# Kernel optimization log

Hardware: AMD Instinct MI355X
Metric: run time of the kernel (lower is better)

Reference implementation:

```python
import jax, jax.numpy as jnp
import numpy as np


def _reverse_padded(x, lengths):
    # x: [T, B, D]; reverse each sequence within its own length (packed-seq semantics)
    T = x.shape[0]
    t = jnp.arange(T)[:, None]                                   # [T, 1]
    idx = jnp.where(t < lengths[None, :], lengths[None, :] - 1 - t, t)  # [T, B]
    return jnp.take_along_axis(x, idx[:, :, None], axis=0)


def _lstm_dir(x, w_ih, w_hh, b):
    # single-direction LSTM, torch gate order (i, f, g, o). x: [T, B, Din]
    T, B, _ = x.shape
    H = w_hh.shape[1]
    xg = jnp.einsum('tbi,gi->tbg', x, w_ih) + b  # precompute input projections [T,B,4H]

    def step(carry, g_x):
        h, c = carry
        g = g_x + h @ w_hh.T
        i, f, gc, o = jnp.split(g, 4, axis=-1)
        c = jax.nn.sigmoid(f) * c + jax.nn.sigmoid(i) * jnp.tanh(gc)
        h = jax.nn.sigmoid(o) * jnp.tanh(c)
        return (h, c), h

    h0 = jnp.zeros((B, H), x.dtype)
    _, hs = jax.lax.scan(step, (h0, h0), xg)
    return hs  # [T, B, H]


def _bilstm_layer(x, lengths, wf, whf, bf, wr, whr, br):
    fwd = _lstm_dir(x, wf, whf, bf)
    rev = _reverse_padded(_lstm_dir(_reverse_padded(x, lengths), wr, whr, br), lengths)
    return jnp.concatenate([fwd, rev], axis=-1)  # [T, B, 2H]


def setup_inputs() -> dict:
    T, B, D, H = 256, 128, 300, 256
    key = jax.random.key(0)
    ks = jax.random.split(key, 24)
    stdv = 1.0 / np.sqrt(H)

    def u(k, shape):
        return jax.random.uniform(k, shape, jnp.float32, -stdv, stdv)

    inp = {
        'x': jax.random.normal(ks[0], (T, B, D), jnp.float32),
        'lengths': jax.random.randint(ks[1], (B,), 1, T + 1),
        # layer 0 forward / reverse
        'w_ih_l0': u(ks[2], (4 * H, D)), 'w_hh_l0': u(ks[3], (4 * H, H)),
        'b_ih_l0': u(ks[4], (4 * H,)), 'b_hh_l0': u(ks[5], (4 * H,)),
        'w_ih_l0r': u(ks[6], (4 * H, D)), 'w_hh_l0r': u(ks[7], (4 * H, H)),
        'b_ih_l0r': u(ks[8], (4 * H,)), 'b_hh_l0r': u(ks[9], (4 * H,)),
        # layer 1 forward / reverse (input dim 2H)
        'w_ih_l1': u(ks[10], (4 * H, 2 * H)), 'w_hh_l1': u(ks[11], (4 * H, H)),
        'b_ih_l1': u(ks[12], (4 * H,)), 'b_hh_l1': u(ks[13], (4 * H,)),
        'w_ih_l1r': u(ks[14], (4 * H, 2 * H)), 'w_hh_l1r': u(ks[15], (4 * H, H)),
        'b_ih_l1r': u(ks[16], (4 * H,)), 'b_hh_l1r': u(ks[17], (4 * H,)),
        # attention MLP + context vector
        'mlp_w': u(ks[18], (2 * H, 2 * H)),
        'mlp_b': u(ks[19], (2 * H,)),
        'ctx': jax.random.normal(ks[20], (2 * H,), jnp.float32) * 0.1,
    }
    return inp


def reference(x, lengths, w_ih_l0, w_hh_l0, b_ih_l0, b_hh_l0,
              w_ih_l0r, w_hh_l0r, b_ih_l0r, b_hh_l0r,
              w_ih_l1, w_hh_l1, b_ih_l1, b_hh_l1,
              w_ih_l1r, w_hh_l1r, b_ih_l1r, b_hh_l1r,
              mlp_w, mlp_b, ctx):
    lengths = jnp.maximum(lengths, 1)
    h1 = _bilstm_layer(x, lengths, w_ih_l0, w_hh_l0, b_ih_l0 + b_hh_l0,
                       w_ih_l0r, w_hh_l0r, b_ih_l0r + b_hh_l0r)
    h2 = _bilstm_layer(h1, lengths, w_ih_l1, w_hh_l1, b_ih_l1 + b_hh_l1,
                       w_ih_l1r, w_hh_l1r, b_ih_l1r + b_hh_l1r)
    out = h2.transpose(1, 0, 2)                                  # [B, T, 2H]
    ann = jnp.tanh(jnp.einsum('btd,ed->bte', out, mlp_w) + mlp_b)  # [B, T, 2H]
    scores = ann @ ctx                                           # [B, T]
    T = out.shape[1]
    mask = jnp.arange(T)[None, :] < lengths[:, None]             # [B, T]
    w = jax.nn.softmax(jnp.where(mask, scores, -1e9), axis=1)    # masked softmax over time
    return jnp.einsum('bt,btd->bd', w, out)                      # [B, 2H]
```

## Files before the change

### kernel.cpp

```cpp
#include <hip/hip_runtime.h>


#define T_ 256
#define B_ 128
#define D_ 300
#define H_ 256
#define G4H 1024
#define H2 512
#define TC 64
#define LDK 40
#define LDA 264

typedef __attribute__((ext_vector_type(8))) short bf16x8;
typedef __attribute__((ext_vector_type(4))) short short4v;
typedef __attribute__((ext_vector_type(4))) float f32x4;

#define MFMA16(a, b, c) __builtin_amdgcn_mfma_f32_16x16x32_bf16(a, b, c, 0, 0, 0)

__device__ __forceinline__ float sigf(float x) { return 1.f / (1.f + __expf(-x)); }
__device__ __forceinline__ float tanhfast(float x) { return 2.f / (1.f + __expf(-2.f * x)) - 1.f; }

__device__ __forceinline__ short hi_bf16(float x) {
  return (short)(__float_as_uint(x) >> 16);
}
__device__ __forceinline__ short lo_bf16(float x) {
  float lo = x - __uint_as_float(__float_as_uint(x) & 0xFFFF0000u);
  return (short)(__float_as_uint(lo) >> 16);
}

__device__ __forceinline__ void split_f4(const float4 v, short* hp, short* lp) {
  short4v h, l;
  h.x = hi_bf16(v.x); l.x = lo_bf16(v.x);
  h.y = hi_bf16(v.y); l.y = lo_bf16(v.y);
  h.z = hi_bf16(v.z); l.z = lo_bf16(v.z);
  h.w = hi_bf16(v.w); l.w = lo_bf16(v.w);
  *(short4v*)hp = h;
  *(short4v*)lp = l;
}

__device__ __forceinline__ void split8(const float4 v0, const float4 v1,
                                       bf16x8* hp, bf16x8* lp) {
  bf16x8 h, l;
  h[0] = hi_bf16(v0.x); l[0] = lo_bf16(v0.x);
  h[1] = hi_bf16(v0.y); l[1] = lo_bf16(v0.y);
  h[2] = hi_bf16(v0.z); l[2] = lo_bf16(v0.z);
  h[3] = hi_bf16(v0.w); l[3] = lo_bf16(v0.w);
  h[4] = hi_bf16(v1.x); l[4] = lo_bf16(v1.x);
  h[5] = hi_bf16(v1.y); l[5] = lo_bf16(v1.y);
  h[6] = hi_bf16(v1.z); l[6] = lo_bf16(v1.z);
  h[7] = hi_bf16(v1.w); l[7] = lo_bf16(v1.w);
  *hp = h; *lp = l;
}

__global__ __launch_bounds__(256, 2) void proj_gemm2(
    const float* __restrict__ X,
    const float* __restrict__ W0, const float* __restrict__ W1,
    const float* __restrict__ b1f, const float* __restrict__ b2f,
    const float* __restrict__ b1r, const float* __restrict__ b2r,
    float* __restrict__ C0, float* __restrict__ C1,
    int N, int K, const int* __restrict__ lengths, int t0)
{
  __shared__ short Xh[128 * LDK], Xl[128 * LDK];
  __shared__ short Wh[128 * LDK], Wl[128 * LDK];
  const int rev = blockIdx.z;
  const float* __restrict__ W = rev ? W1 : W0;
  const float* __restrict__ bias1 = rev ? b1r : b1f;
  const float* __restrict__ bias2 = rev ? b2r : b2f;
  float* __restrict__ C = rev ? C1 : C0;

  const int tid = threadIdx.x;
  const int m0 = blockIdx.y * 128, n0 = blockIdx.x * 128;
  const int s_step = t0 + blockIdx.y;

  const int sr = tid >> 3;
  const int sc = (tid & 7) * 4;
  const float* px[4];
  const float* pw[4];
#pragma unroll
  for (int p = 0; p < 4; p++) {
    const int r = sr + p * 32;
    int ss = s_step;
    if (rev) {
      int lb = lengths[r]; if (lb < 1) lb = 1;
      ss = (s_step < lb) ? (lb - 1 - s_step) : s_step;
    }
    px[p] = X + (size_t)(ss * 128 + r) * K;
    pw[p] = W + (size_t)(n0 + r) * K;
  }

  const int lane = tid & 63, w = tid >> 6;
  const int mb = (w & 1) * 64, nb = (w >> 1) * 64;
  const int r16 = lane & 15, quad = lane >> 4;

  f32x4 acc[4][4];
#pragma unroll
  for (int i = 0; i < 4; i++)
#pragma unroll
    for (int j = 0; j < 4; j++) acc[i][j] = (f32x4){0.f, 0.f, 0.f, 0.f};

  for (int k0 = 0; k0 < K; k0 += 32) {
    const int gk = k0 + sc;
    const bool kin = (gk < K);
#pragma unroll
    for (int p = 0; p < 4; p++) {
      float4 xv = {0.f, 0.f, 0.f, 0.f}, wv = {0.f, 0.f, 0.f, 0.f};
      if (kin) { xv = *(const float4*)(px[p] + gk); wv = *(const float4*)(pw[p] + gk); }
      const int ro = (sr + p * 32) * LDK + sc;
      split_f4(xv, &Xh[ro], &Xl[ro]);
      split_f4(wv, &Wh[ro], &Wl[ro]);
    }
    __syncthreads();

    bf16x8 ah[4], al[4], bh[4], bl[4];
#pragma unroll
    for (int mt = 0; mt < 4; mt++) {
      const int ro = (mb + mt * 16 + r16) * LDK + quad * 8;
      ah[mt] = *(const bf16x8*)&Xh[ro];
      al[mt] = *(const bf16x8*)&Xl[ro];
    }
#pragma unroll
    for (int nt = 0; nt < 4; nt++) {
      const int ro = (nb + nt * 16 + r16) * LDK + quad * 8;
      bh[nt] = *(const bf16x8*)&Wh[ro];
      bl[nt] = *(const bf16x8*)&Wl[ro];
    }
#pragma unroll
    for (int mt = 0; mt < 4; mt++)
#pragma unroll
      for (int nt = 0; nt < 4; nt++) {
        acc[mt][nt] = __builtin_amdgcn_mfma_f32_16x16x32_bf16(ah[mt], bh[nt], acc[mt][nt], 0, 0, 0);
        acc[mt][nt] = __builtin_amdgcn_mfma_f32_16x16x32_bf16(ah[mt], bl[nt], acc[mt][nt], 0, 0, 0);
        acc[mt][nt] = __builtin_amdgcn_mfma_f32_16x16x32_bf16(al[mt], bh[nt], acc[mt][nt], 0, 0, 0);
      }
    __syncthreads();
  }

  float bsum[4];
#pragma unroll
  for (int nt = 0; nt < 4; nt++) {
    const int col = n0 + nb + nt * 16 + r16;
    bsum[nt] = bias1[col] + bias2[col];
  }
#pragma unroll
  for (int mt = 0; mt < 4; mt++) {
    const int row = m0 + mb + mt * 16 + quad * 4;
#pragma unroll
    for (int nt = 0; nt < 4; nt++) {
      const int col = n0 + nb + nt * 16 + r16;
      float* Cp = C + (size_t)row * N + col;
#pragma unroll
      for (int reg = 0; reg < 4; reg++)
        Cp[(size_t)reg * N] = acc[mt][nt][reg] + bsum[nt];
    }
  }
}

__global__ __launch_bounds__(256, 2) void attn_gemm(
    const float* __restrict__ X, const float* __restrict__ W,
    const float* __restrict__ mlp_b, const float* __restrict__ ctx,
    float* __restrict__ scores, int M, int N, int K)
{
  __shared__ short Xh[128 * LDK], Xl[128 * LDK];
  __shared__ short Wh[128 * LDK], Wl[128 * LDK];
  const int tid = threadIdx.x;
  const int m0 = blockIdx.y * 128, n0 = blockIdx.x * 128;

  const int sr = tid >> 3;
  const int sc = (tid & 7) * 4;
  const float* px[4];
  const float* pw[4];
#pragma unroll
  for (int p = 0; p < 4; p++) {
    px[p] = X + (size_t)(m0 + sr + p * 32) * K;
    pw[p] = W + (size_t)(n0 + sr + p * 32) * K;
  }

  const int lane = tid & 63, w = tid >> 6;
  const int mb = (w & 1) * 64, nb = (w >> 1) * 64;
  const int r16 = lane & 15, quad = lane >> 4;

  f32x4 acc[4][4];
#pragma unroll
  for (int i = 0; i < 4; i++)
#pragma unroll
    for (int j = 0; j < 4; j++) acc[i][j] = (f32x4){0.f, 0.f, 0.f, 0.f};

  for (int k0 = 0; k0 < K; k0 += 32) {
    const int gk = k0 + sc;
#pragma unroll
    for (int p = 0; p < 4; p++) {
      float4 xv = *(const float4*)(px[p] + gk);
      float4 wv = *(const float4*)(pw[p] + gk);
      const int ro = (sr + p * 32) * LDK + sc;
      split_f4(xv, &Xh[ro], &Xl[ro]);
      split_f4(wv, &Wh[ro], &Wl[ro]);
    }
    __syncthreads();

    bf16x8 ah[4], al[4], bh[4], bl[4];
#pragma unroll
    for (int mt = 0; mt < 4; mt++) {
      const int ro = (mb + mt * 16 + r16) * LDK + quad * 8;
      ah[mt] = *(const bf16x8*)&Xh[ro];
      al[mt] = *(const bf16x8*)&Xl[ro];
    }
#pragma unroll
    for (int nt = 0; nt < 4; nt++) {
      const int ro = (nb + nt * 16 + r16) * LDK + quad * 8;
      bh[nt] = *(const bf16x8*)&Wh[ro];
      bl[nt] = *(const bf16x8*)&Wl[ro];
    }
#pragma unroll
    for (int mt = 0; mt < 4; mt++)
#pragma unroll
      for (int nt = 0; nt < 4; nt++) {
        acc[mt][nt] = __builtin_amdgcn_mfma_f32_16x16x32_bf16(ah[mt], bh[nt], acc[mt][nt], 0, 0, 0);
        acc[mt][nt] = __builtin_amdgcn_mfma_f32_16x16x32_bf16(ah[mt], bl[nt], acc[mt][nt], 0, 0, 0);
        acc[mt][nt] = __builtin_amdgcn_mfma_f32_16x16x32_bf16(al[mt], bh[nt], acc[mt][nt], 0, 0, 0);
      }
    __syncthreads();
  }

  float bb4[4], cc4[4];
#pragma unroll
  for (int nt = 0; nt < 4; nt++) {
    const int col = n0 + nb + nt * 16 + r16;
    bb4[nt] = mlp_b[col];
    cc4[nt] = ctx[col];
  }
#pragma unroll
  for (int mt = 0; mt < 4; mt++) {
#pragma unroll
    for (int reg = 0; reg < 4; reg++) {
      float ssum = 0.f;
#pragma unroll
      for (int nt = 0; nt < 4; nt++)
        ssum += tanhfast(acc[mt][nt][reg] + bb4[nt]) * cc4[nt];
      ssum += __shfl_xor(ssum, 1);
      ssum += __shfl_xor(ssum, 2);
      ssum += __shfl_xor(ssum, 4);
      ssum += __shfl_xor(ssum, 8);
      if (r16 == 0)
        atomicAdd(&scores[m0 + mb + mt * 16 + quad * 4 + reg], ssum);
    }
  }
}

__global__ __launch_bounds__(256, 1) void lstm_rec(
    const float* __restrict__ xgF, const float* __restrict__ xgR,
    const float* __restrict__ whF, const float* __restrict__ whR,
    const int* __restrict__ lengths, float* __restrict__ hout,
    float* __restrict__ ring, float* __restrict__ bbuf, float* __restrict__ cbuf,
    int t0)
{
  __shared__ short Ah[16 * LDA];
  __shared__ short Al[16 * LDA];
  __shared__ float gbuf[8 * 128];

  const int tid = threadIdx.x;
  const int blk = blockIdx.x;
  const int s = blk >> 5;
  const int d = (blk >> 4) & 1;
  const int g = blk & 15;
  const float* __restrict__ xg = d ? xgR : xgF;
  const float* __restrict__ wh = d ? whR : whF;

  const int lane = tid & 63;
  const int w = tid >> 6;
  const int r16 = lane & 15, quad = lane >> 4;

  const int cb = tid >> 5;
  const int hl = tid & 31;
  const int b = g * 8 + cb;
  const int hdim = s * 32 + hl;
  const int k0 = hl * 8;

  bf16x8 bh[2][8], bl[2][8];
#pragma unroll
  for (int nt = 0; nt < 2; nt++)
#pragma unroll
    for (int kt = 0; kt < 8; kt++) {
      const float* wr = wh + (size_t)(w * 256 + s * 32 + nt * 16 + r16) * 256
                           + kt * 32 + quad * 8;
      float4 v0 = *(const float4*)(wr);
      float4 v1 = *(const float4*)(wr + 4);
      split8(v0, v1, &bh[nt][kt], &bl[nt][kt]);
    }

  {
    int* za = (int*)(Ah + 8 * LDA);
    int* zb = (int*)(Al + 8 * LDA);
    for (int i = tid; i < (8 * LDA) / 2; i += 256) { za[i] = 0; zb[i] = 0; }
  }

  float c;
  if (t0 == 0) {
    int* za = (int*)Ah;
    int* zb = (int*)Al;
    for (int i = tid; i < (8 * LDA) / 2; i += 256) { za[i] = 0; zb[i] = 0; }
    c = 0.f;
  } else {
    const float* src = bbuf + ((size_t)d * 128 + g * 8 + cb) * 256 + k0;
    float4 v0 = *(const float4*)src;
    float4 v1 = *(const float4*)(src + 4);
    bf16x8 hv, lv;
    split8(v0, v1, &hv, &lv);
    *(bf16x8*)&Ah[cb * LDA + k0] = hv;
    *(bf16x8*)&Al[cb * LDA + k0] = lv;
    c = cbuf[((size_t)d * 128 + b) * 256 + hdim];
  }
  int lb = lengths[b]; if (lb < 1) lb = 1;

  const float* xr0 = xg + (size_t)b * 1024 + hdim;
  float x0 = xr0[0], x1 = xr0[256], x2 = xr0[512], x3 = xr0[768];
  __syncthreads();

  const int tend = t0 + TC;
  for (int t = t0; t < tend; t++) {
    const int slot = t - t0;
    const bool last = (t == tend - 1);

    f32x4 aH0 = {0.f,0.f,0.f,0.f}, aM0 = {0.f,0.f,0.f,0.f}, aL0 = {0.f,0.f,0.f,0.f};
    f32x4 aH1 = {0.f,0.f,0.f,0.f}, aM1 = {0.f,0.f,0.f,0.f}, aL1 = {0.f,0.f,0.f,0.f};
#pragma unroll
    for (int kt = 0; kt < 8; kt++) {
      const int ro = r16 * LDA + kt * 32 + quad * 8;
      bf16x8 ahf = *(const bf16x8*)&Ah[ro];
      bf16x8 alf = *(const bf16x8*)&Al[ro];
      aH0 = MFMA16(ahf, bh[0][kt], aH0);
      aM0 = MFMA16(ahf, bl[0][kt], aM0);
      aL0 = MFMA16(alf, bh[0][kt], aL0);
      aH1 = MFMA16(ahf, bh[1][kt], aH1);
      aM1 = MFMA16(ahf, bl[1][kt], aM1);
      aL1 = MFMA16(alf, bh[1][kt], aL1);
    }
    if (quad < 2) {
#pragma unroll
      for (int reg = 0; reg < 4; reg++) {
        gbuf[(quad * 4 + reg) * 128 + w * 32 + r16]      = aH0[reg] + aM0[reg] + aL0[reg];
        gbuf[(quad * 4 + reg) * 128 + w * 32 + 16 + r16] = aH1[reg] + aM1[reg] + aL1[reg];
      }
    }
    __syncthreads();

    const float gi = gbuf[cb * 128 +       hl] + x0;
    const float gf = gbuf[cb * 128 +  32 + hl] + x1;
    const float gg = gbuf[cb * 128 +  64 + hl] + x2;
    const float go = gbuf[cb * 128 +  96 + hl] + x3;
    const float si = sigf(gi), sf = sigf(gf);
    const float tg = tanhfast(gg), so = sigf(go);
    c = sf * c + si * tg;
    const float h = so * tanhfast(c);
    if (!last) {
      __hip_atomic_store(&ring[(((size_t)slot * 2 + d) * 128 + b) * 256 + hdim], h,
                         __ATOMIC_RELAXED, __HIP_MEMORY_SCOPE_AGENT);
    } else {
      bbuf[((size_t)d * 128 + b) * 256 + hdim] = h;
    }
    const int tin = d ? ((t < lb) ? (lb - 1 - t) : t) : t;
    hout[((size_t)tin * 128 + b) * 512 + d * 256 + hdim] = h;

    if (!last) {
      const float* xn = xg + ((size_t)(t + 1 - t0) * 128 + b) * 1024 + hdim;
      const float nx0 = xn[0], nx1 = xn[256], nx2 = xn[512], nx3 = xn[768];

      const unsigned* su = (const unsigned*)(ring +
          (((size_t)slot * 2 + d) * 128 + g * 8 + cb) * 256 + k0);
      unsigned uv[8];
      int it = 0;
      for (;;) {
        bool ok = true;
#pragma unroll
        for (int j = 0; j < 8; j++) {
          uv[j] = __hip_atomic_load(&su[j],
                                    __ATOMIC_RELAXED, __HIP_MEMORY_SCOPE_AGENT);
          ok &= (uv[j] != 0xFFFFFFFFu);
        }
        if (ok || ++it >= 20000) break;
      }
      float4 v0, v1;
      v0.x = __uint_as_float(uv[0]); v0.y = __uint_as_float(uv[1]);
      v0.z = __uint_as_float(uv[2]); v0.w = __uint_as_float(uv[3]);
      v1.x = __uint_as_float(uv[4]); v1.y = __uint_as_float(uv[5]);
      v1.z = __uint_as_float(uv[6]); v1.w = __uint_as_float(uv[7]);
      bf16x8 hv, lv;
      split8(v0, v1, &hv, &lv);
      *(bf16x8*)&Ah[cb * LDA + k0] = hv;
      *(bf16x8*)&Al[cb * LDA + k0] = lv;

      x0 = nx0; x1 = nx1; x2 = nx2; x3 = nx3;
      __syncthreads();
    }
  }
  cbuf[((size_t)d * 128 + b) * 256 + hdim] = c;
}

__global__ __launch_bounds__(256) void attn_final(
    const float* __restrict__ h2, const float* __restrict__ scores,
    const int* __restrict__ lengths, float* __restrict__ out)
{
  __shared__ float sl[256];
  __shared__ float red[256];
  const int b = blockIdx.x, tid = threadIdx.x;
  int lb = lengths[b]; if (lb < 1) lb = 1;
  const float sc = scores[(size_t)tid * 128 + b];
  const bool valid = (tid < lb);
  red[tid] = valid ? sc : -1e30f;
  __syncthreads();
  for (int off = 128; off > 0; off >>= 1) {
    if (tid < off) red[tid] = fmaxf(red[tid], red[tid + off]);
    __syncthreads();
  }
  const float mx = red[0];
  __syncthreads();
  const float p = valid ? __expf(sc - mx) : 0.f;
  red[tid] = p;
  __syncthreads();
  for (int off = 128; off > 0; off >>= 1) {
    if (tid < off) red[tid] += red[tid + off];
    __syncthreads();
  }
  const float inv = 1.f / red[0];
  __syncthreads();
  sl[tid] = p * inv;
  __syncthreads();

  float ax = 0.f, ay = 0.f;
  const int dd = tid * 2;
  for (int t = 0; t < 256; t++) {
    const float w = sl[t];
    if (w != 0.f) {
      const float* row = h2 + ((size_t)t * 128 + b) * 512 + dd;
      ax += w * row[0];
      ay += w * row[1];
    }
  }
  float2 r; r.x = ax; r.y = ay;
  *(float2*)(out + (size_t)b * 512 + dd) = r;
}

extern "C" void kernel_launch(void* const* d_in, const int* in_sizes, int n_in,
                              void* d_out, int out_size, void* d_ws, size_t ws_size,
                              hipStream_t stream) {
  (void)in_sizes; (void)n_in; (void)out_size; (void)ws_size;
  const float* x        = (const float*)d_in[0];
  const int*   lengths  = (const int*)d_in[1];
  const float* w_ih_l0  = (const float*)d_in[2];
  const float* w_hh_l0  = (const float*)d_in[3];
  const float* b_ih_l0  = (const float*)d_in[4];
  const float* b_hh_l0  = (const float*)d_in[5];
  const float* w_ih_l0r = (const float*)d_in[6];
  const float* w_hh_l0r = (const float*)d_in[7];
  const float* b_ih_l0r = (const float*)d_in[8];
  const float* b_hh_l0r = (const float*)d_in[9];
  const float* w_ih_l1  = (const float*)d_in[10];
  const float* w_hh_l1  = (const float*)d_in[11];
  const float* b_ih_l1  = (const float*)d_in[12];
  const float* b_hh_l1  = (const float*)d_in[13];
  const float* w_ih_l1r = (const float*)d_in[14];
  const float* w_hh_l1r = (const float*)d_in[15];
  const float* b_ih_l1r = (const float*)d_in[16];
  const float* b_hh_l1r = (const float*)d_in[17];
  const float* mlp_w    = (const float*)d_in[18];
  const float* mlp_b    = (const float*)d_in[19];
  const float* ctx      = (const float*)d_in[20];
  float* out = (float*)d_out;

  float* ws = (float*)d_ws;
  const size_t XGC    = (size_t)TC * B_ * G4H;
  const size_t H_SZ   = (size_t)T_ * B_ * H2;
  const size_t RINGSZ = (size_t)TC * 2 * B_ * H_;
  float* xgA    = ws;
  float* xgB    = xgA + XGC;
  float* h1     = xgB + XGC;
  float* h2     = h1 + H_SZ;
  float* ring   = h2 + H_SZ;
  float* bbuf   = ring + RINGSZ;
  float* cbuf   = bbuf + 65536;
  float* scores = cbuf + 65536;

  (void)hipMemsetAsync(scores, 0, 32768 * 4, stream);

  dim3 blk(256);
  const dim3 pgrid(G4H / 128, TC, 2);

  for (int c = 0; c < T_ / TC; c++) {
    const int t0 = c * TC;
    proj_gemm2<<<pgrid, blk, 0, stream>>>(x, w_ih_l0, w_ih_l0r,
                                          b_ih_l0, b_hh_l0, b_ih_l0r, b_hh_l0r,
                                          xgA, xgB, G4H, D_, lengths, t0);
    (void)hipMemsetAsync(ring, 0xFF, RINGSZ * 4, stream);
    lstm_rec<<<256, blk, 0, stream>>>(xgA, xgB, w_hh_l0, w_hh_l0r, lengths, h1,
                                      ring, bbuf, cbuf, t0);
  }
  for (int c = 0; c < T_ / TC; c++) {
    const int t0 = c * TC;
    proj_gemm2<<<pgrid, blk, 0, stream>>>(h1, w_ih_l1, w_ih_l1r,
                                          b_ih_l1, b_hh_l1, b_ih_l1r, b_hh_l1r,
                                          xgA, xgB, G4H, H2, lengths, t0);
    (void)hipMemsetAsync(ring, 0xFF, RINGSZ * 4, stream);
    lstm_rec<<<256, blk, 0, stream>>>(xgA, xgB, w_hh_l1, w_hh_l1r, lengths, h2,
                                      ring, bbuf, cbuf, t0);
  }
  attn_gemm<<<dim3(H2 / 128, (T_ * B_) / 128), blk, 0, stream>>>(h2, mlp_w, mlp_b, ctx, scores, T_ * B_, H2, H2);
  attn_final<<<B_, blk, 0, stream>>>(h2, scores, lengths, out);
}
```

Before: 2.385 ms.

## Fuse input projection into persistent LSTM kernel and run all timesteps in one launch

Replaces the four chunked projection-plus-recurrence launches per layer with one projection launch for the first 64 timesteps and one persistent recurrent kernel per layer. That kernel computes the input projections for later timesteps into a 76-slot ring, interleaved with the recurrence. The h exchange ring shrinks to 4 slots, uses a parity bit instead of re-memsetting, and packs the hi/lo bf16 split into one word so readers skip the split. This removes launch overhead, state save/restore and separate GEMM passes, at the cost of extra per-step work on the serial recurrence path and tighter cross-block ordering assumptions.

```diff
diff --git a/kernel.cpp b/kernel.cpp
--- a/kernel.cpp
+++ b/kernel.cpp
@@ -7,15 +7,18 @@
 #define H_ 256
 #define G4H 1024
 #define H2 512
-#define TC 64
 #define LDK 40
 #define LDA 264
+#define XGS 76
+#define RSLOTS 4
 
 typedef __attribute__((ext_vector_type(8))) short bf16x8;
 typedef __attribute__((ext_vector_type(4))) short short4v;
 typedef __attribute__((ext_vector_type(4))) float f32x4;
 
 #define MFMA16(a, b, c) __builtin_amdgcn_mfma_f32_16x16x32_bf16(a, b, c, 0, 0, 0)
+#define ATOM_ST(p, v) __hip_atomic_store((p), (v), __ATOMIC_RELAXED, __HIP_MEMORY_SCOPE_AGENT)
+#define ATOM_LD(p) __hip_atomic_load((p), __ATOMIC_RELAXED, __HIP_MEMORY_SCOPE_AGENT)
 
 __device__ __forceinline__ float sigf(float x) { return 1.f / (1.f + __expf(-x)); }
 __device__ __forceinline__ float tanhfast(float x) { return 2.f / (1.f + __expf(-2.f * x)) - 1.f; }
@@ -246,24 +249,32 @@
   }
 }
 
-__global__ __launch_bounds__(256, 1) void lstm_rec(
-    const float* __restrict__ xgF, const float* __restrict__ xgR,
+__global__ __launch_bounds__(256, 1) void lstm_fused(
+    float* __restrict__ xgF, float* __restrict__ xgR,
+    const float* __restrict__ XSRC,
     const float* __restrict__ whF, const float* __restrict__ whR,
+    const float* __restrict__ wihF, const float* __restrict__ wihR,
+    const float* __restrict__ b1f, const float* __restrict__ b2f,
+    const float* __restrict__ b1r, const float* __restrict__ b2r,
     const int* __restrict__ lengths, float* __restrict__ hout,
-    float* __restrict__ ring, float* __restrict__ bbuf, float* __restrict__ cbuf,
-    int t0)
+    float* __restrict__ ring, int K)
 {
-  __shared__ short Ah[16 * LDA];
-  __shared__ short Al[16 * LDA];
+  __shared__ short Ah[16 * LDA], Al[16 * LDA];
   __shared__ float gbuf[8 * 128];
+  __shared__ short PXh[128 * LDK], PXl[128 * LDK];
+  __shared__ short PWh[128 * LDK], PWl[128 * LDK];
 
   const int tid = threadIdx.x;
   const int blk = blockIdx.x;
   const int s = blk >> 5;
   const int d = (blk >> 4) & 1;
   const int g = blk & 15;
-  const float* __restrict__ xg = d ? xgR : xgF;
+  float* __restrict__ xgd = d ? xgR : xgF;
   const float* __restrict__ wh = d ? whR : whF;
+  const float* __restrict__ wih = d ? wihR : wihF;
+  const float* __restrict__ bias1 = d ? b1r : b1f;
+  const float* __restrict__ bias2 = d ? b2r : b2f;
+  unsigned* __restrict__ ring32 = (unsigned*)ring;
 
   const int lane = tid & 63;
   const int w = tid >> 6;
@@ -274,6 +285,12 @@
   const int b = g * 8 + cb;
   const int hdim = s * 32 + hl;
   const int k0 = hl * 8;
+
+  const int sr = tid >> 3;
+  const int sc = (tid & 7) * 4;
+  const int mb = (w & 1) * 64, nb = (w >> 1) * 64;
+  const int n0 = s * 128;
+  const int KITERS = (K + 31) >> 5;
 
   bf16x8 bh[2][8], bl[2][8];
 #pragma unroll
@@ -287,38 +304,26 @@
       split8(v0, v1, &bh[nt][kt], &bl[nt][kt]);
     }
 
+  f32x4 pacc[4][4];
+#pragma unroll
+  for (int i = 0; i < 4; i++)
+#pragma unroll
+    for (int j = 0; j < 4; j++) pacc[i][j] = (f32x4){0.f, 0.f, 0.f, 0.f};
+
   {
-    int* za = (int*)(Ah + 8 * LDA);
-    int* zb = (int*)(Al + 8 * LDA);
-    for (int i = tid; i < (8 * LDA) / 2; i += 256) { za[i] = 0; zb[i] = 0; }
-  }
-
-  float c;
-  if (t0 == 0) {
     int* za = (int*)Ah;
     int* zb = (int*)Al;
-    for (int i = tid; i < (8 * LDA) / 2; i += 256) { za[i] = 0; zb[i] = 0; }
-    c = 0.f;
-  } else {
-    const float* src = bbuf + ((size_t)d * 128 + g * 8 + cb) * 256 + k0;
-    float4 v0 = *(const float4*)src;
-    float4 v1 = *(const float4*)(src + 4);
-    bf16x8 hv, lv;
-    split8(v0, v1, &hv, &lv);
-    *(bf16x8*)&Ah[cb * LDA + k0] = hv;
-    *(bf16x8*)&Al[cb * LDA + k0] = lv;
-    c = cbuf[((size_t)d * 128 + b) * 256 + hdim];
-  }
+    for (int i = tid; i < (16 * LDA) / 2; i += 256) { za[i] = 0; zb[i] = 0; }
+  }
+  float c = 0.f;
   int lb = lengths[b]; if (lb < 1) lb = 1;
-
-  const float* xr0 = xg + (size_t)b * 1024 + hdim;
-  float x0 = xr0[0], x1 = xr0[256], x2 = xr0[512], x3 = xr0[768];
+  const float* xr0 = xgd + (size_t)b * 1024 + hdim;
+  float x0 = ATOM_LD(xr0), x1 = ATOM_LD(xr0 + 256);
+  float x2 = ATOM_LD(xr0 + 512), x3 = ATOM_LD(xr0 + 768);
   __syncthreads();
 
-  const int tend = t0 + TC;
-  for (int t = t0; t < tend; t++) {
-    const int slot = t - t0;
-    const bool last = (t == tend - 1);
+  for (int t = 0; t < T_; t++) {
+    const bool last = (t == T_ - 1);
 
     f32x4 aH0 = {0.f,0.f,0.f,0.f}, aM0 = {0.f,0.f,0.f,0.f}, aL0 = {0.f,0.f,0.f,0.f};
     f32x4 aH1 = {0.f,0.f,0.f,0.f}, aM1 = {0.f,0.f,0.f,0.f}, aL1 = {0.f,0.f,0.f,0.f};
@@ -352,39 +357,110 @@
     c = sf * c + si * tg;
     const float h = so * tanhfast(c);
     if (!last) {
-      __hip_atomic_store(&ring[(((size_t)slot * 2 + d) * 128 + b) * 256 + hdim], h,
-                         __ATOMIC_RELAXED, __HIP_MEMORY_SCOPE_AGENT);
-    } else {
-      bbuf[((size_t)d * 128 + b) * 256 + hdim] = h;
+      const unsigned hu = (unsigned)(unsigned short)hi_bf16(h);
+      const unsigned lu = (unsigned)(unsigned short)lo_bf16(h);
+      const unsigned pv = (hu << 16) | (lu & 0xFFFEu) | (unsigned)((t >> 2) & 1);
+      ATOM_ST(&ring32[(((t & 3) * 2 + d) * 128 + b) * 256 + hdim], pv);
     }
     const int tin = d ? ((t < lb) ? (lb - 1 - t) : t) : t;
     hout[((size_t)tin * 128 + b) * 512 + d * 256 + hdim] = h;
 
+    if (t < 192) {
+      const int wj = t >> 4, ki = t & 15;
+      const int y = 64 + wj * 16 + g;
+      if (ki < KITERS) {
+        const int gk = ki * 32 + sc;
+        const bool kin = (gk < K);
+#pragma unroll
+        for (int p = 0; p < 4; p++) {
+          const int r = sr + p * 32;
+          float4 xv = {0.f, 0.f, 0.f, 0.f}, wv = {0.f, 0.f, 0.f, 0.f};
+          if (kin) {
+            int ss = y;
+            if (d) {
+              int lbr = lengths[r]; if (lbr < 1) lbr = 1;
+              ss = (y < lbr) ? (lbr - 1 - y) : y;
+            }
+            xv = *(const float4*)(XSRC + ((size_t)ss * 128 + r) * K + gk);
+            wv = *(const float4*)(wih + (size_t)(n0 + r) * K + gk);
+          }
+          const int ro = (sr + p * 32) * LDK + sc;
+          split_f4(xv, &PXh[ro], &PXl[ro]);
+          split_f4(wv, &PWh[ro], &PWl[ro]);
+        }
+        __syncthreads();
+
+        bf16x8 pah[4], pal[4], pbh[4], pbl[4];
+#pragma unroll
+        for (int mt = 0; mt < 4; mt++) {
+          const int ro = (mb + mt * 16 + r16) * LDK + quad * 8;
+          pah[mt] = *(const bf16x8*)&PXh[ro];
+          pal[mt] = *(const bf16x8*)&PXl[ro];
+        }
+#pragma unroll
+        for (int nt = 0; nt < 4; nt++) {
+          const int ro = (nb + nt * 16 + r16) * LDK + quad * 8;
+          pbh[nt] = *(const bf16x8*)&PWh[ro];
+          pbl[nt] = *(const bf16x8*)&PWl[ro];
+        }
+#pragma unroll
+        for (int mt = 0; mt < 4; mt++)
+#pragma unroll
+          for (int nt = 0; nt < 4; nt++) {
+            pacc[mt][nt] = MFMA16(pah[mt], pbh[nt], pacc[mt][nt]);
+            pacc[mt][nt] = MFMA16(pah[mt], pbl[nt], pacc[mt][nt]);
+            pacc[mt][nt] = MFMA16(pal[mt], pbh[nt], pacc[mt][nt]);
+          }
+      }
+      if (ki == 15) {
+        const int yslot = y % XGS;
+        float bsum[4];
+#pragma unroll
+        for (int nt = 0; nt < 4; nt++) {
+          const int col = n0 + nb + nt * 16 + r16;
+          bsum[nt] = bias1[col] + bias2[col];
+        }
+#pragma unroll
+        for (int mt = 0; mt < 4; mt++) {
+          const int row = mb + mt * 16 + quad * 4;
+#pragma unroll
+          for (int nt = 0; nt < 4; nt++) {
+            const int col = n0 + nb + nt * 16 + r16;
+            float* Cp = xgd + ((size_t)yslot * 128 + row) * 1024 + col;
+#pragma unroll
+            for (int reg = 0; reg < 4; reg++)
+              ATOM_ST(&Cp[(size_t)reg * 1024], pacc[mt][nt][reg] + bsum[nt]);
+            pacc[mt][nt] = (f32x4){0.f, 0.f, 0.f, 0.f};
+          }
+        }
+      }
+    }
+
     if (!last) {
-      const float* xn = xg + ((size_t)(t + 1 - t0) * 128 + b) * 1024 + hdim;
-      const float nx0 = xn[0], nx1 = xn[256], nx2 = xn[512], nx3 = xn[768];
-
-      const unsigned* su = (const unsigned*)(ring +
-          (((size_t)slot * 2 + d) * 128 + g * 8 + cb) * 256 + k0);
+      const int ns = (t + 1) % XGS;
+      const float* xn = xgd + ((size_t)ns * 128 + b) * 1024 + hdim;
+      const float nx0 = ATOM_LD(xn), nx1 = ATOM_LD(xn + 256);
+      const float nx2 = ATOM_LD(xn + 512), nx3 = ATOM_LD(xn + 768);
+
+      const unsigned* ru = ring32 + (((t & 3) * 2 + d) * 128 + g * 8 + cb) * 256 + k0;
+      const unsigned par = (unsigned)((t >> 2) & 1);
       unsigned uv[8];
       int it = 0;
       for (;;) {
         bool ok = true;
 #pragma unroll
         for (int j = 0; j < 8; j++) {
-          uv[j] = __hip_atomic_load(&su[j],
-                                    __ATOMIC_RELAXED, __HIP_MEMORY_SCOPE_AGENT);
-          ok &= (uv[j] != 0xFFFFFFFFu);
+          uv[j] = ATOM_LD(&ru[j]);
+          ok &= ((uv[j] & 1u) == par);
         }
-        if (ok || ++it >= 20000) break;
-      }
-      float4 v0, v1;
-      v0.x = __uint_as_float(uv[0]); v0.y = __uint_as_float(uv[1]);
-      v0.z = __uint_as_float(uv[2]); v0.w = __uint_as_float(uv[3]);
-      v1.x = __uint_as_float(uv[4]); v1.y = __uint_as_float(uv[5]);
-      v1.z = __uint_as_float(uv[6]); v1.w = __uint_as_float(uv[7]);
+        if (ok || ++it >= 100000) break;
+      }
       bf16x8 hv, lv;
-      split8(v0, v1, &hv, &lv);
+#pragma unroll
+      for (int j = 0; j < 8; j++) {
+        hv[j] = (short)(uv[j] >> 16);
+        lv[j] = (short)(uv[j] & 0xFFFFu);
+      }
       *(bf16x8*)&Ah[cb * LDA + k0] = hv;
       *(bf16x8*)&Al[cb * LDA + k0] = lv;
 
@@ -392,7 +468,6 @@
       __syncthreads();
     }
   }
-  cbuf[((size_t)d * 128 + b) * 256 + hdim] = c;
 }
 
 __global__ __launch_bounds__(256) void attn_final(
@@ -467,41 +542,37 @@
   float* out = (float*)d_out;
 
   float* ws = (float*)d_ws;
-  const size_t XGC    = (size_t)TC * B_ * G4H;
-  const size_t H_SZ   = (size_t)T_ * B_ * H2;
-  const size_t RINGSZ = (size_t)TC * 2 * B_ * H_;
-  float* xgA    = ws;
-  float* xgB    = xgA + XGC;
-  float* h1     = xgB + XGC;
+  const size_t XG76  = (size_t)XGS * B_ * G4H;
+  const size_t H_SZ  = (size_t)T_ * B_ * H2;
+  const size_t RINGF = (size_t)RSLOTS * 2 * B_ * H_;
+  float* xgF    = ws;
+  float* xgR    = xgF + XG76;
+  float* h1     = xgR + XG76;
   float* h2     = h1 + H_SZ;
   float* ring   = h2 + H_SZ;
-  float* bbuf   = ring + RINGSZ;
-  float* cbuf   = bbuf + 65536;
-  float* scores = cbuf + 65536;
+  float* scores = ring + RINGF;
 
   (void)hipMemsetAsync(scores, 0, 32768 * 4, stream);
 
   dim3 blk(256);
-  const dim3 pgrid(G4H / 128, TC, 2);
-
-  for (int c = 0; c < T_ / TC; c++) {
-    const int t0 = c * TC;
-    proj_gemm2<<<pgrid, blk, 0, stream>>>(x, w_ih_l0, w_ih_l0r,
-                                          b_ih_l0, b_hh_l0, b_ih_l0r, b_hh_l0r,
-                                          xgA, xgB, G4H, D_, lengths, t0);
-    (void)hipMemsetAsync(ring, 0xFF, RINGSZ * 4, stream);
-    lstm_rec<<<256, blk, 0, stream>>>(xgA, xgB, w_hh_l0, w_hh_l0r, lengths, h1,
-                                      ring, bbuf, cbuf, t0);
-  }
-  for (int c = 0; c < T_ / TC; c++) {
-    const int t0 = c * TC;
-    proj_gemm2<<<pgrid, blk, 0, stream>>>(h1, w_ih_l1, w_ih_l1r,
-                                          b_ih_l1, b_hh_l1, b_ih_l1r, b_hh_l1r,
-                                          xgA, xgB, G4H, H2, lengths, t0);
-    (void)hipMemsetAsync(ring, 0xFF, RINGSZ * 4, stream);
-    lstm_rec<<<256, blk, 0, stream>>>(xgA, xgB, w_hh_l1, w_hh_l1r, lengths, h2,
-                                      ring, bbuf, cbuf, t0);
-  }
+  const dim3 pgrid(G4H / 128, 64, 2);
+
+  proj_gemm2<<<pgrid, blk, 0, stream>>>(x, w_ih_l0, w_ih_l0r,
+                                        b_ih_l0, b_hh_l0, b_ih_l0r, b_hh_l0r,
+                                        xgF, xgR, G4H, D_, lengths, 0);
+  (void)hipMemsetAsync(ring, 0xFF, RINGF * 4, stream);
+  lstm_fused<<<256, blk, 0, stream>>>(xgF, xgR, x, w_hh_l0, w_hh_l0r,
+                                      w_ih_l0, w_ih_l0r,
+                                      b_ih_l0, b_hh_l0, b_ih_l0r, b_hh_l0r,
+                                      lengths, h1, ring, D_);
+  proj_gemm2<<<pgrid, blk, 0, stream>>>(h1, w_ih_l1, w_ih_l1r,
+                                        b_ih_l1, b_hh_l1, b_ih_l1r, b_hh_l1r,
+                                        xgF, xgR, G4H, H2, lengths, 0);
+  (void)hipMemsetAsync(ring, 0xFF, RINGF * 4, stream);
+  lstm_fused<<<256, blk, 0, stream>>>(xgF, xgR, h1, w_hh_l1, w_hh_l1r,
+                                      w_ih_l1, w_ih_l1r,
+                                      b_ih_l1, b_hh_l1, b_ih_l1r, b_hh_l1r,
+                                      lengths, h2, ring, H2);
   attn_gemm<<<dim3(H2 / 128, (T_ * B_) / 128), blk, 0, stream>>>(h2, mlp_w, mlp_b, ctx, scores, T_ * B_, H2, H2);
   attn_final<<<B_, blk, 0, stream>>>(h2, scores, lengths, out);
 }
```

New measurement: 2.639 ms. +10.6%, slower.
